# Performance work log

Measured on AMD Instinct MI355X. Metric: run time of the kernel, lower is better.

Reference implementation:

```python
import jax, jax.numpy as jnp
import numpy as np

NUM_ENT = 14541
NUM_REL = 474
D = 400
B = 32
N_CAND = 14505


def setup_inputs() -> dict:
    key = jax.random.key(0)
    k0, k1, k2, k4, k5 = jax.random.split(key, 5)
    return {
        "arg0_1": jax.random.normal(k0, (NUM_ENT, D), dtype=jnp.float32),   # entity embeddings
        "arg1_1": jax.random.normal(k1, (NUM_REL, D), dtype=jnp.float32),   # relation centers
        "arg2_1": jax.random.uniform(k2, (NUM_REL, D), dtype=jnp.float32),  # relation offsets (box widths)
        "arg3_1": jnp.ones((1,), dtype=jnp.float32),                        # margin gamma
        "arg4_1": jax.random.randint(k4, (B, 2), 0, NUM_REL),               # (head_id, rel_id) pairs
        "arg5_1": jax.random.randint(k5, (4, N_CAND), 0, NUM_ENT),          # candidate entity ids (row 0 used)
    }


def reference(arg0_1, arg1_1, arg2_1, arg3_1, arg4_1, arg5_1):
    # Gather heads / relation params
    head = arg0_1[arg4_1[:, 0]]            # [B, D]
    rel_c = arg1_1[arg4_1[:, 1]]           # [B, D]
    rel_o = arg2_1[arg4_1[:, 1]]           # [B, D]

    query = (head + rel_c)[:, None, :]     # [B, 1, D] box center
    offset = rel_o[:, None, :]             # [B, 1, D] box width

    # Candidate tail embeddings: only row 0 of arg5_1 is used in the graph
    cand = arg0_1[arg5_1[0].reshape(-1)][None, :, :]  # [1, N_CAND, D]

    d = jnp.abs(cand - query)                           # [B, N_CAND, D]
    dist_outside = jax.nn.relu(d - offset).sum(-1)      # [B, N_CAND]
    dist_inside = jnp.abs(jnp.minimum(d, offset)).sum(-1)

    return arg3_1 - dist_outside - 0.02 * dist_inside   # [B, N_CAND]
```

## Files before the change

### kernel.cpp

```cpp
#include <hip/hip_runtime.h>

#define DIM     400
#define B       32
#define NCAND   14505
#define NROUND  3627
#define TSTRIPS 256
#define THREADS 256

__global__ __launch_bounds__(THREADS, 2)
void score_kernel(const float* __restrict__ ent,
                  const float* __restrict__ relc,
                  const float* __restrict__ relo,
                  const float* __restrict__ onev,
                  const int*   __restrict__ pairs,
                  const int*   __restrict__ cidx,
                  float* __restrict__ out) {
    const int fid  = blockIdx.x;
    const int xcd  = fid & 7;
    const int rest = fid >> 3;
    const int bq   = rest & 7;
    const int tc   = rest >> 3;
    const int t    = xcd + 8 * tc;

    const int tid  = threadIdx.x;
    const int lane = tid & 63;
    const int u    = lane & 15;
    const int g    = lane >> 4;
    const int b    = __builtin_amdgcn_readfirstlane(bq * 4 + (tid >> 6));

    const int hd = pairs[b * 2 + 0];
    const int rl = pairs[b * 2 + 1];
    const float4* hb = (const float4*)(ent  + (size_t)hd * DIM) + u;
    const float4* cb = (const float4*)(relc + (size_t)rl * DIM) + u;
    const float4* ob = (const float4*)(relo + (size_t)rl * DIM) + u;

    float4 q[7], o[7];
    float oa = 0.f;
#pragma unroll
    for (int k = 0; k < 6; ++k) {
        float4 h = hb[16 * k], c = cb[16 * k];
        q[k] = make_float4(h.x + c.x, h.y + c.y, h.z + c.z, h.w + c.w);
        o[k] = ob[16 * k];
        oa += o[k].x + o[k].y + o[k].z + o[k].w;
    }
    if (u < 4) {
        float4 h = hb[96], c = cb[96];
        q[6] = make_float4(h.x + c.x, h.y + c.y, h.z + c.z, h.w + c.w);
        o[6] = ob[96];
        oa += o[6].x + o[6].y + o[6].z + o[6].w;
    }
    oa += __shfl_xor(oa, 1);
    oa += __shfl_xor(oa, 2);
    oa += __shfl_xor(oa, 4);
    oa += __shfl_xor(oa, 8);
    const float base = onev[0] + 0.98f * oa;

    const float4* entu = (const float4*)ent + u;

    for (int rr = t; rr < NROUND; rr += TSTRIPS) {
        const int cand = 4 * rr + g;
        const int ci   = cidx[cand < NCAND ? cand : NCAND - 1];
        const float4* p = entu + (size_t)ci * 100;

        float4 cbuf[7];
#pragma unroll
        for (int k = 0; k < 6; ++k) cbuf[k] = p[16 * k];
        if (u < 4) cbuf[6] = p[96];

        float am0 = 0.f, ad0 = 0.f, am1 = 0.f, ad1 = 0.f;
#define E(vc, vq, vo, AM, AD)                     \
        {                                         \
            float d_ = (vc) - (vq);               \
            AM += fmaxf(fabsf(d_), (vo));         \
            AD += fabsf(d_);                      \
        }
#define F4(k, AM, AD)                             \
        E(cbuf[k].x, q[k].x, o[k].x, AM, AD)      \
        E(cbuf[k].y, q[k].y, o[k].y, AM, AD)      \
        E(cbuf[k].z, q[k].z, o[k].z, AM, AD)      \
        E(cbuf[k].w, q[k].w, o[k].w, AM, AD)

        F4(0, am0, ad0) F4(1, am1, ad1)
        F4(2, am0, ad0) F4(3, am1, ad1)
        F4(4, am0, ad0) F4(5, am1, ad1)
        if (u < 4) { F4(6, am0, ad0) }
#undef F4
#undef E

        float s_ = fmaf(-0.98f, am0 + am1, -0.02f * (ad0 + ad1));
        s_ += __shfl_xor(s_, 1);
        s_ += __shfl_xor(s_, 2);
        s_ += __shfl_xor(s_, 4);
        s_ += __shfl_xor(s_, 8);

        if (u == 0 && cand < NCAND)
            out[(size_t)b * NCAND + cand] = base + s_;
    }
}

extern "C" void kernel_launch(void* const* d_in, const int* in_sizes, int n_in,
                              void* d_out, int out_size, void* d_ws, size_t ws_size,
                              hipStream_t stream) {
    const float* ent   = (const float*)d_in[0];
    const float* relc  = (const float*)d_in[1];
    const float* relo  = (const float*)d_in[2];
    const float* onev  = (const float*)d_in[3];
    const int*   pairs = (const int*)d_in[4];
    const int*   cidx  = (const int*)d_in[5];
    float*       out   = (float*)d_out;

    const int grid = 8 * 8 * 32;
    score_kernel<<<grid, THREADS, 0, stream>>>(ent, relc, relo, onev, pairs, cidx, out);
}
```

Baseline: 46.16 us.

## Share candidate rows across batch queries via cross-lane shuffle rotation

Each wavefront now holds four different batch queries, one per 16-lane group, and loads four candidate rows. It rotates those rows among the groups with xor shuffles so every query scores every loaded candidate. This divides global candidate loads per score by four, and the grid is halved to match. The cost is 112 extra shuffles per round and per-lane query registers that are no longer wave-uniform, which may increase register pressure.

```diff
diff --git a/kernel.cpp b/kernel.cpp
--- a/kernel.cpp
+++ b/kernel.cpp
@@ -4,7 +4,7 @@
 #define B       32
 #define NCAND   14505
 #define NROUND  3627
-#define TSTRIPS 256
+#define NSTRIP  512
 #define THREADS 256
 
 __global__ __launch_bounds__(THREADS, 2)
@@ -18,15 +18,15 @@
     const int fid  = blockIdx.x;
     const int xcd  = fid & 7;
     const int rest = fid >> 3;
-    const int bq   = rest & 7;
-    const int tc   = rest >> 3;
-    const int t    = xcd + 8 * tc;
-
+    const int w    = rest & 7;
+    const int sc   = rest >> 3;
     const int tid  = threadIdx.x;
+    const int wid  = tid >> 6;
     const int lane = tid & 63;
     const int u    = lane & 15;
     const int g    = lane >> 4;
-    const int b    = __builtin_amdgcn_readfirstlane(bq * 4 + (tid >> 6));
+    const int strip = xcd + 8 * (4 * sc + wid);
+    const int b    = 4 * w + g;
 
     const int hd = pairs[b * 2 + 0];
     const int rl = pairs[b * 2 + 1];
@@ -57,17 +57,6 @@
 
     const float4* entu = (const float4*)ent + u;
 
-    for (int rr = t; rr < NROUND; rr += TSTRIPS) {
-        const int cand = 4 * rr + g;
-        const int ci   = cidx[cand < NCAND ? cand : NCAND - 1];
-        const float4* p = entu + (size_t)ci * 100;
-
-        float4 cbuf[7];
-#pragma unroll
-        for (int k = 0; k < 6; ++k) cbuf[k] = p[16 * k];
-        if (u < 4) cbuf[6] = p[96];
-
-        float am0 = 0.f, ad0 = 0.f, am1 = 0.f, ad1 = 0.f;
 #define E(vc, vq, vo, AM, AD)                     \
         {                                         \
             float d_ = (vc) - (vq);               \
@@ -80,22 +69,57 @@
         E(cbuf[k].z, q[k].z, o[k].z, AM, AD)      \
         E(cbuf[k].w, q[k].w, o[k].w, AM, AD)
 
-        F4(0, am0, ad0) F4(1, am1, ad1)
-        F4(2, am0, ad0) F4(3, am1, ad1)
-        F4(4, am0, ad0) F4(5, am1, ad1)
-        if (u < 4) { F4(6, am0, ad0) }
+#define PHASE(m)                                                   \
+    {                                                              \
+        float am0 = 0.f, ad0 = 0.f, am1 = 0.f, ad1 = 0.f;          \
+        F4(0, am0, ad0) F4(1, am1, ad1)                            \
+        F4(2, am0, ad0) F4(3, am1, ad1)                            \
+        F4(4, am0, ad0) F4(5, am1, ad1)                            \
+        if (u < 4) { F4(6, am0, ad0) }                             \
+        float s_ = fmaf(-0.98f, am0 + am1, -0.02f * (ad0 + ad1));  \
+        s_ += __shfl_xor(s_, 1);                                   \
+        s_ += __shfl_xor(s_, 2);                                   \
+        s_ += __shfl_xor(s_, 4);                                   \
+        s_ += __shfl_xor(s_, 8);                                   \
+        const int cand_ = cq + (g ^ (m));                          \
+        if (u == 0 && cand_ < NCAND)                               \
+            out[(size_t)b * NCAND + cand_] = base + s_;            \
+    }
+
+#define ROT(mask)                                                  \
+    {                                                              \
+        _Pragma("unroll")                                          \
+        for (int k = 0; k < 7; ++k) {                              \
+            cbuf[k].x = __shfl_xor(cbuf[k].x, mask);               \
+            cbuf[k].y = __shfl_xor(cbuf[k].y, mask);               \
+            cbuf[k].z = __shfl_xor(cbuf[k].z, mask);               \
+            cbuf[k].w = __shfl_xor(cbuf[k].w, mask);               \
+        }                                                          \
+    }
+
+    for (int rr = strip; rr < NROUND; rr += NSTRIP) {
+        const int cq  = 4 * rr;
+        const int cl  = cq + g;
+        const int ci  = cidx[cl < NCAND ? cl : NCAND - 1];
+        const float4* p = entu + (size_t)ci * 100;
+
+        float4 cbuf[7];
+#pragma unroll
+        for (int k = 0; k < 6; ++k) cbuf[k] = p[16 * k];
+        if (u < 4) cbuf[6] = p[96];
+
+        PHASE(0)
+        ROT(16)
+        PHASE(1)
+        ROT(32)
+        PHASE(3)
+        ROT(16)
+        PHASE(2)
+    }
+#undef ROT
+#undef PHASE
 #undef F4
 #undef E
-
-        float s_ = fmaf(-0.98f, am0 + am1, -0.02f * (ad0 + ad1));
-        s_ += __shfl_xor(s_, 1);
-        s_ += __shfl_xor(s_, 2);
-        s_ += __shfl_xor(s_, 4);
-        s_ += __shfl_xor(s_, 8);
-
-        if (u == 0 && cand < NCAND)
-            out[(size_t)b * NCAND + cand] = base + s_;
-    }
 }
 
 extern "C" void kernel_launch(void* const* d_in, const int* in_sizes, int n_in,
@@ -109,6 +133,6 @@
     const int*   cidx  = (const int*)d_in[5];
     float*       out   = (float*)d_out;
 
-    const int grid = 8 * 8 * 32;
+    const int grid = 8 * 8 * 16;
     score_kernel<<<grid, THREADS, 0, stream>>>(ent, relc, relo, onev, pairs, cidx, out);
 }
```

Result: slower. 50.44 us (+9.3%).

## Score two queries per wave to reuse each gathered candidate row

Applied to the files above, without the earlier changes.

Each wave now handles two batch queries (b0 and b0+4) for every candidate row it gathers, so each entity-row load is reused twice. The grid shrinks to 512 blocks with 128 strips. The launch-bounds occupancy hint is dropped to leave room for the doubled per-query registers. The aim is to halve gather traffic and L2 pressure, at the cost of higher register use and fewer waves to hide latency.

```diff
diff --git a/kernel.cpp b/kernel.cpp
--- a/kernel.cpp
+++ b/kernel.cpp
@@ -4,10 +4,10 @@
 #define B       32
 #define NCAND   14505
 #define NROUND  3627
-#define TSTRIPS 256
+#define NSTRIP  128
 #define THREADS 256
 
-__global__ __launch_bounds__(THREADS, 2)
+__global__ __launch_bounds__(THREADS)
 void score_kernel(const float* __restrict__ ent,
                   const float* __restrict__ relc,
                   const float* __restrict__ relo,
@@ -18,48 +18,81 @@
     const int fid  = blockIdx.x;
     const int xcd  = fid & 7;
     const int rest = fid >> 3;
-    const int bq   = rest & 7;
-    const int tc   = rest >> 3;
-    const int t    = xcd + 8 * tc;
+    const int beta = rest & 3;
+    const int sc   = rest >> 2;
+    const int strip = xcd + 8 * sc;
 
     const int tid  = threadIdx.x;
+    const int wid  = tid >> 6;
     const int lane = tid & 63;
     const int u    = lane & 15;
     const int g    = lane >> 4;
-    const int b    = __builtin_amdgcn_readfirstlane(bq * 4 + (tid >> 6));
 
-    const int hd = pairs[b * 2 + 0];
-    const int rl = pairs[b * 2 + 1];
-    const float4* hb = (const float4*)(ent  + (size_t)hd * DIM) + u;
-    const float4* cb = (const float4*)(relc + (size_t)rl * DIM) + u;
-    const float4* ob = (const float4*)(relo + (size_t)rl * DIM) + u;
+    const int b0 = __builtin_amdgcn_readfirstlane(8 * beta + wid);
+    const int b1 = b0 + 4;
 
-    float4 q[7], o[7];
-    float oa = 0.f;
+    const int h0 = pairs[b0 * 2 + 0], r0 = pairs[b0 * 2 + 1];
+    const int h1 = pairs[b1 * 2 + 0], r1 = pairs[b1 * 2 + 1];
+    const float4* h0p = (const float4*)(ent  + (size_t)h0 * DIM) + u;
+    const float4* c0p = (const float4*)(relc + (size_t)r0 * DIM) + u;
+    const float4* o0p = (const float4*)(relo + (size_t)r0 * DIM) + u;
+    const float4* h1p = (const float4*)(ent  + (size_t)h1 * DIM) + u;
+    const float4* c1p = (const float4*)(relc + (size_t)r1 * DIM) + u;
+    const float4* o1p = (const float4*)(relo + (size_t)r1 * DIM) + u;
+
+    float4 q0[7], o0[7], q1[7], o1[7];
+    float oa0 = 0.f, oa1 = 0.f;
 #pragma unroll
     for (int k = 0; k < 6; ++k) {
-        float4 h = hb[16 * k], c = cb[16 * k];
-        q[k] = make_float4(h.x + c.x, h.y + c.y, h.z + c.z, h.w + c.w);
-        o[k] = ob[16 * k];
-        oa += o[k].x + o[k].y + o[k].z + o[k].w;
+        float4 h = h0p[16 * k], c = c0p[16 * k];
+        q0[k] = make_float4(h.x + c.x, h.y + c.y, h.z + c.z, h.w + c.w);
+        o0[k] = o0p[16 * k];
+        oa0 += o0[k].x + o0[k].y + o0[k].z + o0[k].w;
+        h = h1p[16 * k]; c = c1p[16 * k];
+        q1[k] = make_float4(h.x + c.x, h.y + c.y, h.z + c.z, h.w + c.w);
+        o1[k] = o1p[16 * k];
+        oa1 += o1[k].x + o1[k].y + o1[k].z + o1[k].w;
     }
     if (u < 4) {
-        float4 h = hb[96], c = cb[96];
-        q[6] = make_float4(h.x + c.x, h.y + c.y, h.z + c.z, h.w + c.w);
-        o[6] = ob[96];
-        oa += o[6].x + o[6].y + o[6].z + o[6].w;
+        float4 h = h0p[96], c = c0p[96];
+        q0[6] = make_float4(h.x + c.x, h.y + c.y, h.z + c.z, h.w + c.w);
+        o0[6] = o0p[96];
+        oa0 += o0[6].x + o0[6].y + o0[6].z + o0[6].w;
+        h = h1p[96]; c = c1p[96];
+        q1[6] = make_float4(h.x + c.x, h.y + c.y, h.z + c.z, h.w + c.w);
+        o1[6] = o1p[96];
+        oa1 += o1[6].x + o1[6].y + o1[6].z + o1[6].w;
     }
-    oa += __shfl_xor(oa, 1);
-    oa += __shfl_xor(oa, 2);
-    oa += __shfl_xor(oa, 4);
-    oa += __shfl_xor(oa, 8);
-    const float base = onev[0] + 0.98f * oa;
+    oa0 += __shfl_xor(oa0, 1); oa1 += __shfl_xor(oa1, 1);
+    oa0 += __shfl_xor(oa0, 2); oa1 += __shfl_xor(oa1, 2);
+    oa0 += __shfl_xor(oa0, 4); oa1 += __shfl_xor(oa1, 4);
+    oa0 += __shfl_xor(oa0, 8); oa1 += __shfl_xor(oa1, 8);
+    const float onec  = onev[0];
+    const float base0 = onec + 0.98f * oa0;
+    const float base1 = onec + 0.98f * oa1;
 
     const float4* entu = (const float4*)ent + u;
 
-    for (int rr = t; rr < NROUND; rr += TSTRIPS) {
-        const int cand = 4 * rr + g;
-        const int ci   = cidx[cand < NCAND ? cand : NCAND - 1];
+#define E(vc, vq, vo, AM, AD)                     \
+        {                                         \
+            float d_ = (vc) - (vq);               \
+            AM += fmaxf(fabsf(d_), (vo));         \
+            AD += fabsf(d_);                      \
+        }
+#define F4(k)                                                   \
+        E(cbuf[k].x, q0[k].x, o0[k].x, am0, ad0)                \
+        E(cbuf[k].x, q1[k].x, o1[k].x, am1, ad1)                \
+        E(cbuf[k].y, q0[k].y, o0[k].y, am0, ad0)                \
+        E(cbuf[k].y, q1[k].y, o1[k].y, am1, ad1)                \
+        E(cbuf[k].z, q0[k].z, o0[k].z, am0, ad0)                \
+        E(cbuf[k].z, q1[k].z, o1[k].z, am1, ad1)                \
+        E(cbuf[k].w, q0[k].w, o0[k].w, am0, ad0)                \
+        E(cbuf[k].w, q1[k].w, o1[k].w, am1, ad1)
+
+    for (int rr = strip; rr < NROUND; rr += NSTRIP) {
+        const int cq = 4 * rr;
+        const int cl = cq + g;
+        const int ci = cidx[cl < NCAND ? cl : NCAND - 1];
         const float4* p = entu + (size_t)ci * 100;
 
         float4 cbuf[7];
@@ -68,34 +101,23 @@
         if (u < 4) cbuf[6] = p[96];
 
         float am0 = 0.f, ad0 = 0.f, am1 = 0.f, ad1 = 0.f;
-#define E(vc, vq, vo, AM, AD)                     \
-        {                                         \
-            float d_ = (vc) - (vq);               \
-            AM += fmaxf(fabsf(d_), (vo));         \
-            AD += fabsf(d_);                      \
+        F4(0) F4(1) F4(2) F4(3) F4(4) F4(5)
+        if (u < 4) { F4(6) }
+
+        float s0 = fmaf(-0.98f, am0, -0.02f * ad0);
+        float s1 = fmaf(-0.98f, am1, -0.02f * ad1);
+        s0 += __shfl_xor(s0, 1); s1 += __shfl_xor(s1, 1);
+        s0 += __shfl_xor(s0, 2); s1 += __shfl_xor(s1, 2);
+        s0 += __shfl_xor(s0, 4); s1 += __shfl_xor(s1, 4);
+        s0 += __shfl_xor(s0, 8); s1 += __shfl_xor(s1, 8);
+
+        if (u == 0 && cl < NCAND) {
+            out[(size_t)b0 * NCAND + cl] = base0 + s0;
+            out[(size_t)b1 * NCAND + cl] = base1 + s1;
         }
-#define F4(k, AM, AD)                             \
-        E(cbuf[k].x, q[k].x, o[k].x, AM, AD)      \
-        E(cbuf[k].y, q[k].y, o[k].y, AM, AD)      \
-        E(cbuf[k].z, q[k].z, o[k].z, AM, AD)      \
-        E(cbuf[k].w, q[k].w, o[k].w, AM, AD)
-
-        F4(0, am0, ad0) F4(1, am1, ad1)
-        F4(2, am0, ad0) F4(3, am1, ad1)
-        F4(4, am0, ad0) F4(5, am1, ad1)
-        if (u < 4) { F4(6, am0, ad0) }
+    }
 #undef F4
 #undef E
-
-        float s_ = fmaf(-0.98f, am0 + am1, -0.02f * (ad0 + ad1));
-        s_ += __shfl_xor(s_, 1);
-        s_ += __shfl_xor(s_, 2);
-        s_ += __shfl_xor(s_, 4);
-        s_ += __shfl_xor(s_, 8);
-
-        if (u == 0 && cand < NCAND)
-            out[(size_t)b * NCAND + cand] = base + s_;
-    }
 }
 
 extern "C" void kernel_launch(void* const* d_in, const int* in_sizes, int n_in,
@@ -109,6 +131,6 @@
     const int*   cidx  = (const int*)d_in[5];
     float*       out   = (float*)d_out;
 
-    const int grid = 8 * 8 * 32;
+    const int grid = 8 * 4 * 16;
     score_kernel<<<grid, THREADS, 0, stream>>>(ent, relc, relo, onev, pairs, cidx, out);
 }
```

Result: no change. 46.50 us (+0.7%).

## Convert entity table to fp16 and score candidates with packed half math

Applied to the files above, without the earlier changes.

Adds a pre-pass that converts the full entity table to fp16 in workspace, plus a small prep kernel that precomputes the fp16 query centers, pre-scaled offsets and the per-query base constant. The scoring kernel then gathers half-width candidate rows and uses packed-half subtract/abs/max with dot2 accumulation into fp32, after rewriting the two sums as a single max term. The aim is to halve the gathered bytes and the per-element ALU work. In exchange it re-reads and rewrites the whole table on every call, adds two extra launches, and loses precision from fp16 rounding. It falls back to the fp32 path when the workspace is too small.

```diff
diff --git a/kernel.cpp b/kernel.cpp
--- a/kernel.cpp
+++ b/kernel.cpp
@@ -1,20 +1,156 @@
 #include <hip/hip_runtime.h>
 
 #define DIM     400
+#define NENT    14541
 #define B       32
 #define NCAND   14505
 #define NROUND  3627
 #define TSTRIPS 256
 #define THREADS 256
 
+typedef __attribute__((ext_vector_type(2))) _Float16 half2_t;
+
+static __device__ __forceinline__ half2_t bch(unsigned u) {
+    return __builtin_bit_cast(half2_t, u);
+}
+static __device__ __forceinline__ half2_t habs2(half2_t x) {
+    unsigned u = __builtin_bit_cast(unsigned, x) & 0x7fff7fffu;
+    return __builtin_bit_cast(half2_t, u);
+}
+static __device__ __forceinline__ unsigned pkh(float x, float y) {
+    half2_t h;
+    h.x = (_Float16)x;
+    h.y = (_Float16)y;
+    return __builtin_bit_cast(unsigned, h);
+}
+static __device__ __forceinline__ float dot2acc(half2_t m, float s) {
+#if __has_builtin(__builtin_amdgcn_fdot2)
+    const half2_t ones = {(_Float16)1.f, (_Float16)1.f};
+    return __builtin_amdgcn_fdot2(m, ones, s, false);
+#else
+    return s + (float)m.x + (float)m.y;
+#endif
+}
+
+__global__ void cvt_kernel(const float* __restrict__ ent, uint4* __restrict__ dst) {
+    const int TOT8 = NENT * DIM / 8;
+    int i = blockIdx.x * THREADS + threadIdx.x;
+    if (i >= TOT8) return;
+    const float4* s4 = (const float4*)ent;
+    float4 a = s4[2 * i], b = s4[2 * i + 1];
+    uint4 o;
+    o.x = pkh(a.x, a.y);
+    o.y = pkh(a.z, a.w);
+    o.z = pkh(b.x, b.y);
+    o.w = pkh(b.z, b.w);
+    dst[i] = o;
+}
+
+__global__ void prep_kernel(const float* __restrict__ ent,
+                            const float* __restrict__ relc,
+                            const float* __restrict__ relo,
+                            const float* __restrict__ onev,
+                            const int*   __restrict__ pairs,
+                            _Float16* __restrict__ q16,
+                            _Float16* __restrict__ o16,
+                            float* __restrict__ baseg) {
+    const int b   = blockIdx.x;
+    const int tid = threadIdx.x;
+    const int h = pairs[2 * b + 0];
+    const int r = pairs[2 * b + 1];
+    float so = 0.f;
+    for (int i = tid; i < DIM; i += THREADS) {
+        float qv = ent[(size_t)h * DIM + i] + relc[(size_t)r * DIM + i];
+        float ov = relo[(size_t)r * DIM + i];
+        q16[(size_t)b * DIM + i] = (_Float16)qv;
+        o16[(size_t)b * DIM + i] = (_Float16)(0.98f * ov);
+        so += ov;
+    }
+    __shared__ float sred[4];
+    for (int off = 32; off; off >>= 1) so += __shfl_down(so, off);
+    if ((tid & 63) == 0) sred[tid >> 6] = so;
+    __syncthreads();
+    if (tid == 0)
+        baseg[b] = onev[0] + 0.98f * (sred[0] + sred[1] + sred[2] + sred[3]);
+}
+
 __global__ __launch_bounds__(THREADS, 2)
-void score_kernel(const float* __restrict__ ent,
-                  const float* __restrict__ relc,
-                  const float* __restrict__ relo,
-                  const float* __restrict__ onev,
-                  const int*   __restrict__ pairs,
-                  const int*   __restrict__ cidx,
-                  float* __restrict__ out) {
+void score_f16(const uint4* __restrict__ ent16,
+               const uint4* __restrict__ q16,
+               const uint4* __restrict__ o16,
+               const float* __restrict__ baseg,
+               const int*   __restrict__ cidx,
+               float* __restrict__ out) {
+    const int fid  = blockIdx.x;
+    const int xcd  = fid & 7;
+    const int rest = fid >> 3;
+    const int bq   = rest & 7;
+    const int tc   = rest >> 3;
+    const int t    = xcd + 8 * tc;
+
+    const int tid  = threadIdx.x;
+    const int lane = tid & 63;
+    const int u    = lane & 15;
+    const int g    = lane >> 4;
+    const int b    = __builtin_amdgcn_readfirstlane(bq * 4 + (tid >> 6));
+
+    const uint4* qb = q16 + (size_t)b * 50;
+    const uint4* ob = o16 + (size_t)b * 50;
+    uint4 qr0 = qb[u], qr1 = qb[u + 16], qr2 = qb[u + 32];
+    uint4 or0 = ob[u], or1 = ob[u + 16], or2 = ob[u + 32];
+    uint4 qr3 = qr0, or3 = or0;
+    if (u < 2) { qr3 = qb[48 + u]; or3 = ob[48 + u]; }
+    const float base = baseg[b];
+
+    const half2_t K002 = {(_Float16)0.02f, (_Float16)0.02f};
+
+#define PAIR(cu, qu, ou)                                        \
+    {                                                           \
+        half2_t cc_ = bch(cu), qq_ = bch(qu), oo_ = bch(ou);    \
+        half2_t dd_ = cc_ - qq_;                                \
+        half2_t aa_ = habs2(dd_);                               \
+        half2_t ee_ = aa_ * K002 + oo_;                         \
+        half2_t mm_ = __builtin_elementwise_max(aa_, ee_);      \
+        s = dot2acc(mm_, s);                                    \
+    }
+#define PROC(C, Q, O) \
+    PAIR(C.x, Q.x, O.x) PAIR(C.y, Q.y, O.y) PAIR(C.z, Q.z, O.z) PAIR(C.w, Q.w, O.w)
+
+    for (int rr = t; rr < NROUND; rr += TSTRIPS) {
+        const int cand = 4 * rr + g;
+        const int ci   = cidx[cand < NCAND ? cand : NCAND - 1];
+        const uint4* p = ent16 + (size_t)ci * 50;
+
+        uint4 cv0 = p[u], cv1 = p[u + 16], cv2 = p[u + 32];
+        uint4 cv3;
+        if (u < 2) cv3 = p[48 + u];
+
+        float s = 0.f;
+        PROC(cv0, qr0, or0)
+        PROC(cv1, qr1, or1)
+        PROC(cv2, qr2, or2)
+        if (u < 2) { PROC(cv3, qr3, or3) }
+
+        s += __shfl_xor(s, 1);
+        s += __shfl_xor(s, 2);
+        s += __shfl_xor(s, 4);
+        s += __shfl_xor(s, 8);
+
+        if (u == 0 && cand < NCAND)
+            out[(size_t)b * NCAND + cand] = base - s;
+    }
+#undef PROC
+#undef PAIR
+}
+
+__global__ __launch_bounds__(THREADS, 2)
+void score_f32(const float* __restrict__ ent,
+               const float* __restrict__ relc,
+               const float* __restrict__ relo,
+               const float* __restrict__ onev,
+               const int*   __restrict__ pairs,
+               const int*   __restrict__ cidx,
+               float* __restrict__ out) {
     const int fid  = blockIdx.x;
     const int xcd  = fid & 7;
     const int rest = fid >> 3;
@@ -57,17 +193,6 @@
 
     const float4* entu = (const float4*)ent + u;
 
-    for (int rr = t; rr < NROUND; rr += TSTRIPS) {
-        const int cand = 4 * rr + g;
-        const int ci   = cidx[cand < NCAND ? cand : NCAND - 1];
-        const float4* p = entu + (size_t)ci * 100;
-
-        float4 cbuf[7];
-#pragma unroll
-        for (int k = 0; k < 6; ++k) cbuf[k] = p[16 * k];
-        if (u < 4) cbuf[6] = p[96];
-
-        float am0 = 0.f, ad0 = 0.f, am1 = 0.f, ad1 = 0.f;
 #define E(vc, vq, vo, AM, AD)                     \
         {                                         \
             float d_ = (vc) - (vq);               \
@@ -80,12 +205,21 @@
         E(cbuf[k].z, q[k].z, o[k].z, AM, AD)      \
         E(cbuf[k].w, q[k].w, o[k].w, AM, AD)
 
+    for (int rr = t; rr < NROUND; rr += TSTRIPS) {
+        const int cand = 4 * rr + g;
+        const int ci   = cidx[cand < NCAND ? cand : NCAND - 1];
+        const float4* p = entu + (size_t)ci * 100;
+
+        float4 cbuf[7];
+#pragma unroll
+        for (int k = 0; k < 6; ++k) cbuf[k] = p[16 * k];
+        if (u < 4) cbuf[6] = p[96];
+
+        float am0 = 0.f, ad0 = 0.f, am1 = 0.f, ad1 = 0.f;
         F4(0, am0, ad0) F4(1, am1, ad1)
         F4(2, am0, ad0) F4(3, am1, ad1)
         F4(4, am0, ad0) F4(5, am1, ad1)
         if (u < 4) { F4(6, am0, ad0) }
-#undef F4
-#undef E
 
         float s_ = fmaf(-0.98f, am0 + am1, -0.02f * (ad0 + ad1));
         s_ += __shfl_xor(s_, 1);
@@ -96,6 +230,8 @@
         if (u == 0 && cand < NCAND)
             out[(size_t)b * NCAND + cand] = base + s_;
     }
+#undef F4
+#undef E
 }
 
 extern "C" void kernel_launch(void* const* d_in, const int* in_sizes, int n_in,
@@ -109,6 +245,24 @@
     const int*   cidx  = (const int*)d_in[5];
     float*       out   = (float*)d_out;
 
+    const size_t entB = (size_t)NENT * DIM * 2;
+    const size_t qB   = (size_t)B * DIM * 2;
+    const size_t need = entB + 2 * qB + B * sizeof(float);
     const int grid = 8 * 8 * 32;
-    score_kernel<<<grid, THREADS, 0, stream>>>(ent, relc, relo, onev, pairs, cidx, out);
-}
+
+    if (ws_size >= need) {
+        unsigned char* w = (unsigned char*)d_ws;
+        uint4*    ent16 = (uint4*)w;
+        _Float16* q16   = (_Float16*)(w + entB);
+        _Float16* o16   = (_Float16*)(w + entB + qB);
+        float*    baseg = (float*)(w + entB + 2 * qB);
+
+        const int TOT8 = NENT * DIM / 8;
+        cvt_kernel<<<(TOT8 + THREADS - 1) / THREADS, THREADS, 0, stream>>>(ent, ent16);
+        prep_kernel<<<B, THREADS, 0, stream>>>(ent, relc, relo, onev, pairs, q16, o16, baseg);
+        score_f16<<<grid, THREADS, 0, stream>>>(
+            ent16, (const uint4*)q16, (const uint4*)o16, baseg, cidx, out);
+    } else {
+        score_f32<<<grid, THREADS, 0, stream>>>(ent, relc, relo, onev, pairs, cidx, out);
+    }
+}
```

Measured after the change: 45.87 us. Within noise of the previous version (-0.6%).
